# Kernel tuning notes

Hardware: AMD Instinct MI355X
Metric: run time of the kernel (lower is better)

## Reference

```python
import jax, jax.numpy as jnp
import numpy as np

PLANE_SIZE = 512
FEATURE_DIM = 8
N_LEVELS = 8
MULTISCALE = [1, 2, 4]
LOG2_PS = 9.0  # log2(plane_size)
N_SAMPLES = 1 << 20


def _build_pyramid(tex):
    # tex: [3, R, R, C] -> (flat [3, T, C], sizes [L], offsets [L]) via 2x2 box-filter mips
    levels = [tex]
    t = tex
    for _ in range(N_LEVELS - 1):
        P, h, w, C = t.shape
        t = t.reshape(P, h // 2, 2, w // 2, 2, C).mean(axis=(2, 4))
        levels.append(t)
    sizes = np.array([l.shape[1] for l in levels], dtype=np.int32)
    offsets = np.array([0] + list(np.cumsum(sizes.astype(np.int64) ** 2)[:-1]), dtype=np.int32)
    flat = jnp.concatenate([l.reshape(l.shape[0], -1, l.shape[-1]) for l in levels], axis=1)
    return flat, jnp.asarray(sizes), jnp.asarray(offsets)


def _bilinear_at_level(flat, sizes, offsets, uv, lvl_idx):
    # flat: [3, T, C]; uv: [3, N, 2] in [0,1]; lvl_idx: [3, N] int32
    szi = sizes[lvl_idx]                      # [3, N]
    sz = szi.astype(uv.dtype)
    px = uv[..., 0] * sz - 0.5                # texel centers at (i+0.5)/sz
    py = uv[..., 1] * sz - 0.5
    x0 = jnp.floor(px)
    y0 = jnp.floor(py)
    fx = (px - x0)[..., None]
    fy = (py - y0)[..., None]
    x0i = jnp.clip(x0.astype(jnp.int32), 0, szi - 1)
    x1i = jnp.clip(x0.astype(jnp.int32) + 1, 0, szi - 1)
    y0i = jnp.clip(y0.astype(jnp.int32), 0, szi - 1)
    y1i = jnp.clip(y0.astype(jnp.int32) + 1, 0, szi - 1)
    base = offsets[lvl_idx]

    def gather(yi, xi):
        idx = base + yi * szi + xi            # [3, N]
        return jax.vmap(lambda t, i: t[i])(flat, idx)  # [3, N, C]

    v00 = gather(y0i, x0i)
    v01 = gather(y0i, x1i)
    v10 = gather(y1i, x0i)
    v11 = gather(y1i, x1i)
    top = v00 * (1.0 - fx) + v01 * fx
    bot = v10 * (1.0 - fx) + v11 * fx
    return top * (1.0 - fy) + bot * fy


def _texture(grid, uv, bias):
    # mip-biased trilinear lookup (nvdiffrast linear-mipmap-linear, clamp boundary)
    flat, sizes, offsets = _build_pyramid(grid)
    max_mip = N_LEVELS - 1
    lvl = jnp.clip(bias, 0.0, float(max_mip))
    l0 = jnp.floor(lvl).astype(jnp.int32)
    l1 = jnp.minimum(l0 + 1, max_mip)
    f = (lvl - l0.astype(lvl.dtype))[..., None]
    s0 = _bilinear_at_level(flat, sizes, offsets, uv, l0)
    s1 = _bilinear_at_level(flat, sizes, offsets, uv, l1)
    return s0 * (1.0 - f) + s1 * f            # [3, N, C]


def _forward(x, level, grids):
    n = x.shape[0]
    uv = jnp.stack([x[:, [1, 2]], x[:, [0, 2]], x[:, [0, 1]]], axis=0)  # [3, N, 2]
    lvl = jnp.broadcast_to(level[:, 0][None, :], (3, n))                # [3, N]
    outs = []
    for s, g in enumerate(grids):
        enc = _texture(g, uv, lvl + LOG2_PS + float(s))                 # [3, N, C]
        outs.append(jnp.transpose(enc, (1, 0, 2)).reshape(n, 3 * FEATURE_DIM))
    return jnp.concatenate(outs, axis=-1)     # [N, 3*C*n_scales]


def setup_inputs() -> dict:
    key = jax.random.key(0)
    ks = jax.random.split(key, 5)
    x = jax.random.uniform(ks[0], (N_SAMPLES, 3), dtype=jnp.float32)
    # per-sample LOD so that bias = level + log2(plane_size) + scale spans the mip pyramid
    level = jax.random.uniform(ks[1], (N_SAMPLES, 1), dtype=jnp.float32) * (N_LEVELS - 1) - LOG2_PS
    inp = {"x": x, "level": level}
    for s, mult in enumerate(MULTISCALE):
        r = PLANE_SIZE * mult
        inp[f"grid{s}"] = jax.random.uniform(ks[2 + s], (3, r, r, FEATURE_DIM), jnp.float32, -0.01, 0.01)
    return inp


def reference(x, level, grid0, grid1, grid2):
    return _forward(x, level, (grid0, grid1, grid2))
```

## Files before the change

kernel.cpp:

```cpp
#include <hip/hip_runtime.h>

#define BLK 256
#define SBLK 192
#define NBIN 4096
#define NB 256


#define T0 0
#define T1 1048560
#define T2 2097072
#define TEX_TOTAL 3145392

__device__ __forceinline__ unsigned bfrne(float x) {
    unsigned u = __float_as_uint(x);
    return (u + 0x7fffu + ((u >> 16) & 1u)) >> 16;
}

__device__ __forceinline__ uint4 pack8(const float o[8]) {
    uint4 q;
    q.x = bfrne(o[0]) | (bfrne(o[1]) << 16);
    q.y = bfrne(o[2]) | (bfrne(o[3]) << 16);
    q.z = bfrne(o[4]) | (bfrne(o[5]) << 16);
    q.w = bfrne(o[6]) | (bfrne(o[7]) << 16);
    return q;
}

__device__ __forceinline__ void dec8(const uint4 q, float o[8]) {
    o[0] = __uint_as_float(q.x << 16);
    o[1] = __uint_as_float(q.x & 0xffff0000u);
    o[2] = __uint_as_float(q.y << 16);
    o[3] = __uint_as_float(q.y & 0xffff0000u);
    o[4] = __uint_as_float(q.z << 16);
    o[5] = __uint_as_float(q.z & 0xffff0000u);
    o[6] = __uint_as_float(q.w << 16);
    o[7] = __uint_as_float(q.w & 0xffff0000u);
}

__device__ __forceinline__ void acc8(const uint4 q, float w, float o[8]) {
    o[0] = fmaf(__uint_as_float(q.x << 16), w, o[0]);
    o[1] = fmaf(__uint_as_float(q.x & 0xffff0000u), w, o[1]);
    o[2] = fmaf(__uint_as_float(q.y << 16), w, o[2]);
    o[3] = fmaf(__uint_as_float(q.y & 0xffff0000u), w, o[3]);
    o[4] = fmaf(__uint_as_float(q.z << 16), w, o[4]);
    o[5] = fmaf(__uint_as_float(q.z & 0xffff0000u), w, o[5]);
    o[6] = fmaf(__uint_as_float(q.w << 16), w, o[6]);
    o[7] = fmaf(__uint_as_float(q.w & 0xffff0000u), w, o[7]);
}

__device__ __forceinline__ unsigned spread3(unsigned v) {
    return (v & 1u) | ((v & 2u) << 2) | ((v & 4u) << 4);
}

__device__ __forceinline__ unsigned mkey(float a, float b, float c, float lev) {
    int il = (int)(lev + 9.0f); il = min(max(il, 0), 7);
    int ia = (int)(a * 8.0f); ia = min(max(ia, 0), 7);
    int ib = (int)(b * 8.0f); ib = min(max(ib, 0), 7);
    int ic = (int)(c * 8.0f); ic = min(max(ic, 0), 7);
    unsigned m = (spread3((unsigned)ia) << 2) | (spread3((unsigned)ib) << 1) | spread3((unsigned)ic);
    return (m << 3) | (unsigned)il;
}

__global__ void __launch_bounds__(BLK) base_hist_kernel(
    const float* __restrict__ g0, const float* __restrict__ g1,
    const float* __restrict__ g2, uint4* __restrict__ wsT,
    const float* __restrict__ x, const float* __restrict__ level,
    unsigned* __restrict__ counts,
    int bA, int bB, int bC, int bBase, int n, int chunk) {
    if ((int)blockIdx.x >= bBase) {
        __shared__ unsigned h[NBIN];
        for (int b = threadIdx.x; b < NBIN; b += BLK) h[b] = 0;
        __syncthreads();
        int blk = blockIdx.x - bBase;
        int lo = blk * chunk, hi = min(lo + chunk, n);
        for (int i = lo + (int)threadIdx.x; i < hi; i += BLK) {
            unsigned key = mkey(x[3 * i], x[3 * i + 1], x[3 * i + 2], level[i]);
            atomicAdd(&h[key], 1u);
        }
        __syncthreads();
        for (int b = threadIdx.x; b < NBIN; b += BLK)
            counts[(size_t)b * NB + blk] = h[b];
        return;
    }
    int j = blockIdx.x * BLK + threadIdx.x;
    if (j >= bC) return;
    if (j < bA) {
        const float4* sp = (const float4*)g0 + (size_t)j * 2;
        float4 a = sp[0], b = sp[1];
        float o[8] = {a.x, a.y, a.z, a.w, b.x, b.y, b.z, b.w};
        wsT[T0 + j] = pack8(o);
    } else if (j < bB) {
        int t = j - bA;
        int p = t >> 18;
        int rem = t & ((1 << 18) - 1);
        int y = rem >> 9;
        int x2 = rem & 511;
        const float4* sp = (const float4*)g1 + (size_t)p * 1024 * 1024 * 2;
        float o[8] = {0, 0, 0, 0, 0, 0, 0, 0};
#pragma unroll
        for (int dy = 0; dy < 2; ++dy) {
#pragma unroll
            for (int dx = 0; dx < 2; ++dx) {
                size_t idx = ((size_t)(2 * y + dy) * 1024 + (2 * x2 + dx)) * 2;
                float4 a = sp[idx], b = sp[idx + 1];
                o[0] += a.x; o[1] += a.y; o[2] += a.z; o[3] += a.w;
                o[4] += b.x; o[5] += b.y; o[6] += b.z; o[7] += b.w;
            }
        }
#pragma unroll
        for (int c = 0; c < 8; ++c) o[c] *= 0.25f;
        wsT[T1 + t] = pack8(o);
    } else {
        int t = j - bB;
        int p = t >> 18;
        int rem = t & ((1 << 18) - 1);
        int y = rem >> 9;
        int x2 = rem & 511;
        const float4* sp = (const float4*)g2 + (size_t)p * 2048 * 2048 * 2;
        float o[8] = {0, 0, 0, 0, 0, 0, 0, 0};
#pragma unroll
        for (int dy = 0; dy < 4; ++dy) {
#pragma unroll
            for (int dx = 0; dx < 4; ++dx) {
                size_t idx = ((size_t)(4 * y + dy) * 2048 + (4 * x2 + dx)) * 2;
                float4 a = sp[idx], b = sp[idx + 1];
                o[0] += a.x; o[1] += a.y; o[2] += a.z; o[3] += a.w;
                o[4] += b.x; o[5] += b.y; o[6] += b.z; o[7] += b.w;
            }
        }
#pragma unroll
        for (int c = 0; c < 8; ++c) o[c] *= 0.0625f;
        wsT[T2 + t] = pack8(o);
    }
}

__global__ void __launch_bounds__(BLK) down2b_kernel(
    uint4* __restrict__ wsT,
    int srcA, int dstA, int lszA, int bA,
    int srcB, int dstB, int lszB, int bB,
    int srcC, int dstC, int lszC, int bC) {
    int j = blockIdx.x * BLK + threadIdx.x;
    if (j >= bC) return;
    int src, dst, lsz;
    if (j < bA) {
        src = srcA; dst = dstA; lsz = lszA;
    } else if (j < bB) {
        src = srcB; dst = dstB; lsz = lszB; j -= bA;
    } else {
        src = srcC; dst = dstC; lsz = lszC; j -= bB;
    }
    int sz = 1 << lsz;
    int p = j >> (2 * lsz);
    int rem = j & (sz * sz - 1);
    int y = rem >> lsz;
    int x = rem & (sz - 1);
    int S = sz << 1;
    const uint4* sp = wsT + src + (size_t)p * S * S;
    size_t i00 = (size_t)(2 * y) * S + 2 * x;
    float d0[8], d1[8], d2[8], d3[8];
    dec8(sp[i00], d0);
    dec8(sp[i00 + 1], d1);
    dec8(sp[i00 + S], d2);
    dec8(sp[i00 + S + 1], d3);
    float o[8];
#pragma unroll
    for (int c = 0; c < 8; ++c) o[c] = (d0[c] + d1[c] + d2[c] + d3[c]) * 0.25f;
    wsT[dst + (size_t)(p << (2 * lsz)) + rem] = pack8(o);
}

__global__ void __launch_bounds__(NB) scanA_kernel(
    unsigned* __restrict__ counts, unsigned* __restrict__ binTotal) {
    __shared__ unsigned tmp[NB];
    int bin = blockIdx.x, t = threadIdx.x;
    unsigned v = counts[(size_t)bin * NB + t];
    tmp[t] = v;
    __syncthreads();
    for (int d = 1; d < NB; d <<= 1) {
        unsigned u = (t >= d) ? tmp[t - d] : 0u;
        __syncthreads();
        tmp[t] += u;
        __syncthreads();
    }
    counts[(size_t)bin * NB + t] = tmp[t] - v;
    if (t == NB - 1) binTotal[bin] = tmp[t];
}

__global__ void __launch_bounds__(1024) scanB_kernel(
    const unsigned* __restrict__ binTotal, unsigned* __restrict__ binBase) {
    __shared__ unsigned tmp[1024];
    int t = threadIdx.x;
    unsigned v0 = binTotal[4 * t];
    unsigned v1 = binTotal[4 * t + 1];
    unsigned v2 = binTotal[4 * t + 2];
    unsigned v3 = binTotal[4 * t + 3];
    unsigned sum = v0 + v1 + v2 + v3;
    tmp[t] = sum;
    __syncthreads();
    for (int d = 1; d < 1024; d <<= 1) {
        unsigned u = (t >= d) ? tmp[t - d] : 0u;
        __syncthreads();
        tmp[t] += u;
        __syncthreads();
    }
    unsigned base = tmp[t] - sum;
    binBase[4 * t] = base;
    binBase[4 * t + 1] = base + v0;
    binBase[4 * t + 2] = base + v0 + v1;
    binBase[4 * t + 3] = base + v0 + v1 + v2;
}

__global__ void __launch_bounds__(BLK) scatter_kernel(
    const float* __restrict__ x, const float* __restrict__ level,
    const unsigned* __restrict__ prefix, const unsigned* __restrict__ binBase,
    float4* __restrict__ xs, unsigned* __restrict__ perm, int n, int chunk) {
    __shared__ unsigned h[NBIN];
    for (int b = threadIdx.x; b < NBIN; b += BLK) h[b] = 0;
    __syncthreads();
    int blk = blockIdx.x;
    int lo = blk * chunk, hi = min(lo + chunk, n);
    for (int i = lo + (int)threadIdx.x; i < hi; i += BLK) {
        float a = x[3 * i], b = x[3 * i + 1], c = x[3 * i + 2];
        float lv = level[i];
        unsigned key = mkey(a, b, c, lv);
        unsigned r = atomicAdd(&h[key], 1u);
        unsigned pos = binBase[key] + prefix[(size_t)key * NB + blk] + r;
        xs[pos] = make_float4(a, b, c, lv);
        perm[pos] = (unsigned)i;
    }
}

__device__ __forceinline__ void addr4(const uint4* __restrict__ t, int sz,
                                      float u, float v,
                                      const uint4** a, float* w) {
    float fsz = (float)sz;
    float px = u * fsz - 0.5f;
    float py = v * fsz - 0.5f;
    float x0f = floorf(px), y0f = floorf(py);
    float fx = px - x0f, fy = py - y0f;
    int xi = (int)x0f, yi = (int)y0f;
    int m = sz - 1;
    int x0 = min(max(xi, 0), m);
    int x1 = min(max(xi + 1, 0), m);
    int y0 = min(max(yi, 0), m);
    int y1 = min(max(yi + 1, 0), m);
    const uint4* r0 = t + (size_t)y0 * sz;
    const uint4* r1 = t + (size_t)y1 * sz;
    a[0] = r0 + x0;
    a[1] = r0 + x1;
    a[2] = r1 + x0;
    a[3] = r1 + x1;
    w[0] = (1.0f - fx) * (1.0f - fy);
    w[1] = fx * (1.0f - fy);
    w[2] = (1.0f - fx) * fy;
    w[3] = fx * fy;
}

__global__ void __launch_bounds__(SBLK) tex_sample_kernel(
    const float4* __restrict__ xs, const unsigned* __restrict__ perm,
    const uint4* __restrict__ wsT, float* __restrict__ out, int n) {
    __shared__ float so[3][64][25];
    __shared__ unsigned soi[64];
    int nblk = gridDim.x;
    int cpx = nblk >> 3;
    int bid = blockIdx.x;
    int bswz = (bid & 7) * cpx + (bid >> 3);
    int lane = threadIdx.x & 63;
    int s = threadIdx.x >> 6;
    int base = bswz * 64;
    int j = base + lane;
    bool valid = j < n;

    if (valid) {
        float4 xl = xs[j];
        float xv0 = xl.x, xv1 = xl.y, xv2 = xl.z, lev = xl.w;
        if (s == 0) soi[lane] = perm[j];

        const int WSS_[3] = {T0, T1, T2};
        const int OFFMIN_[3] = {0, 1048576, 5242880};

        const int R = 512 << s;
        float bias = lev + 9.0f + (float)s;
        float lvl = fminf(fmaxf(bias, 0.0f), 7.0f);
        float l0f = floorf(lvl);
        int l0 = (int)l0f;
        int l1 = min(l0 + 1, 7);
        float f = lvl - l0f;
        int sz0 = R >> l0;
        int sz1 = R >> l1;
        int off0 = ((R * R - sz0 * sz0) * 4) / 3;
        int off1 = ((R * R - sz1 * sz1) * 4) / 3;
        const uint4* base0 = wsT + WSS_[s] + (size_t)3 * (off0 - OFFMIN_[s]);
        const uint4* base1 = wsT + WSS_[s] + (size_t)3 * (off1 - OFFMIN_[s]);

        const uint4* ap[24];
        float w[6][4];
#pragma unroll
        for (int p = 0; p < 3; ++p) {
            float u = (p == 0) ? xv1 : xv0;
            float v = (p == 2) ? xv1 : xv2;
            addr4(base0 + (size_t)p * (sz0 * sz0), sz0, u, v, &ap[8 * p], w[2 * p]);
            addr4(base1 + (size_t)p * (sz1 * sz1), sz1, u, v, &ap[8 * p + 4], w[2 * p + 1]);
        }
        uint4 q[24];
#pragma unroll
        for (int t = 0; t < 24; ++t) q[t] = *ap[t];

        float omf = 1.0f - f;
#pragma unroll
        for (int p = 0; p < 3; ++p) {
            float a[8] = {0, 0, 0, 0, 0, 0, 0, 0};
            float b[8] = {0, 0, 0, 0, 0, 0, 0, 0};
#pragma unroll
            for (int t = 0; t < 4; ++t) acc8(q[8 * p + t], w[2 * p][t], a);
#pragma unroll
            for (int t = 0; t < 4; ++t) acc8(q[8 * p + 4 + t], w[2 * p + 1][t], b);
#pragma unroll
            for (int c = 0; c < 8; ++c)
                so[s][lane][8 * p + c] = a[c] * omf + b[c] * f;
        }
    }
    __syncthreads();
    if (valid) {
#pragma unroll
        for (int k = 0; k < 6; ++k) {
            int e = k * 64 + lane;
            int sample = (e * 10923) >> 16;
            int word = e - 6 * sample;
            if (base + sample < n) {
                float4 v;
                v.x = so[s][sample][word * 4 + 0];
                v.y = so[s][sample][word * 4 + 1];
                v.z = so[s][sample][word * 4 + 2];
                v.w = so[s][sample][word * 4 + 3];
                *(float4*)(out + (size_t)soi[sample] * 72 + s * 24 + word * 4) = v;
            }
        }
    }
}

extern "C" void kernel_launch(void* const* d_in, const int* in_sizes, int n_in,
                              void* d_out, int out_size, void* d_ws, size_t ws_size,
                              hipStream_t stream) {
    const float* x = (const float*)d_in[0];
    const float* level = (const float*)d_in[1];
    const float* g0 = (const float*)d_in[2];
    const float* g1 = (const float*)d_in[3];
    const float* g2 = (const float*)d_in[4];
    float* out = (float*)d_out;
    uint4* wsT = (uint4*)d_ws;
    int n = in_sizes[0] / 3;

    float4* xs = (float4*)(wsT + TEX_TOTAL);
    unsigned* perm = (unsigned*)(xs + n);
    unsigned* counts = perm + n;
    unsigned* binTotal = counts + (size_t)NBIN * NB;
    unsigned* binBase = binTotal + NBIN;

    auto lvlOff = [](int s, int l) -> int {
        const int WSS[3] = {T0, T1, T2};
        const int OFFMIN[3] = {0, 1048576, 5242880};
        int R = 512 << s;
        int sz = R >> l;
        int off = ((R * R - sz * sz) * 4) / 3;
        return WSS[s] + 3 * (off - OFFMIN[s]);
    };

    int chunk = (n + NB - 1) / NB;

    {
        int bA = 3 * 512 * 512;
        int bB = bA * 2;
        int bC = bA * 3;
        int bBase = (bC + BLK - 1) / BLK;
        base_hist_kernel<<<bBase + NB, BLK, 0, stream>>>(
            g0, g1, g2, wsT, x, level, counts, bA, bB, bC, bBase, n, chunk);
    }
    for (int l = 1; l <= 7; ++l) {
        int szA = 512 >> l;
        int bA = 3 * szA * szA;
        int srcA = lvlOff(0, l - 1), dstA = lvlOff(0, l), lszA = 9 - l;
        int bB = bA, srcB = 0, dstB = 0, lszB = 0;
        int bC = bA, srcC = 0, dstC = 0, lszC = 0;
        if (l >= 2) {
            int szB = 1024 >> l;
            bB = bA + 3 * szB * szB;
            srcB = lvlOff(1, l - 1); dstB = lvlOff(1, l); lszB = 10 - l;
            bC = bB;
        }
        if (l >= 3) {
            int szC = 2048 >> l;
            bC = bB + 3 * szC * szC;
            srcC = lvlOff(2, l - 1); dstC = lvlOff(2, l); lszC = 11 - l;
        }
        down2b_kernel<<<(bC + BLK - 1) / BLK, BLK, 0, stream>>>(
            wsT, srcA, dstA, lszA, bA, srcB, dstB, lszB, bB, srcC, dstC, lszC, bC);
    }

    scanA_kernel<<<NBIN, NB, 0, stream>>>(counts, binTotal);
    scanB_kernel<<<1, 1024, 0, stream>>>(binTotal, binBase);
    scatter_kernel<<<NB, BLK, 0, stream>>>(x, level, counts, binBase, xs, perm, n, chunk);

    int nblk = (n + 63) / 64;
    nblk = (nblk + 7) & ~7;
    tex_sample_kernel<<<nblk, SBLK, 0, stream>>>(xs, perm, wsT, out, n);
}
```

Before: 412.6 us.

## Fuse mip downsample levels into scan/scatter kernels; split sampler per plane

```diff
diff --git a/kernel.cpp b/kernel.cpp
--- a/kernel.cpp
+++ b/kernel.cpp
@@ -1,7 +1,7 @@
 #include <hip/hip_runtime.h>
 
 #define BLK 256
-#define SBLK 192
+#define SBLK 576
 #define NBIN 4096
 #define NB 256
 
@@ -133,12 +133,11 @@
     }
 }
 
-__global__ void __launch_bounds__(BLK) down2b_kernel(
-    uint4* __restrict__ wsT,
+__device__ __forceinline__ void down2b_body(
+    uint4* __restrict__ wsT, int j,
     int srcA, int dstA, int lszA, int bA,
     int srcB, int dstB, int lszB, int bB,
     int srcC, int dstC, int lszC, int bC) {
-    int j = blockIdx.x * BLK + threadIdx.x;
     if (j >= bC) return;
     int src, dst, lsz;
     if (j < bA) {
@@ -167,65 +166,104 @@
     wsT[dst + (size_t)(p << (2 * lsz)) + rem] = pack8(o);
 }
 
-__global__ void __launch_bounds__(NB) scanA_kernel(
-    unsigned* __restrict__ counts, unsigned* __restrict__ binTotal) {
-    __shared__ unsigned tmp[NB];
-    int bin = blockIdx.x, t = threadIdx.x;
-    unsigned v = counts[(size_t)bin * NB + t];
-    tmp[t] = v;
-    __syncthreads();
-    for (int d = 1; d < NB; d <<= 1) {
-        unsigned u = (t >= d) ? tmp[t - d] : 0u;
+__global__ void __launch_bounds__(BLK) down2b_kernel(
+    uint4* __restrict__ wsT,
+    int srcA, int dstA, int lszA, int bA,
+    int srcB, int dstB, int lszB, int bB,
+    int srcC, int dstC, int lszC, int bC) {
+    down2b_body(wsT, blockIdx.x * BLK + threadIdx.x,
+                srcA, dstA, lszA, bA, srcB, dstB, lszB, bB, srcC, dstC, lszC, bC);
+}
+
+__global__ void __launch_bounds__(BLK) scanA_down_kernel(
+    uint4* __restrict__ wsT, unsigned* __restrict__ counts,
+    unsigned* __restrict__ binTotal, int nScan,
+    int srcA, int dstA, int lszA, int bA,
+    int srcB, int dstB, int lszB, int bB,
+    int srcC, int dstC, int lszC, int bC) {
+    if ((int)blockIdx.x < nScan) {
+        __shared__ unsigned tmp[NB];
+        int bin = blockIdx.x, t = threadIdx.x;
+        unsigned v = counts[(size_t)bin * NB + t];
+        tmp[t] = v;
         __syncthreads();
-        tmp[t] += u;
+        for (int d = 1; d < NB; d <<= 1) {
+            unsigned u = (t >= d) ? tmp[t - d] : 0u;
+            __syncthreads();
+            tmp[t] += u;
+            __syncthreads();
+        }
+        counts[(size_t)bin * NB + t] = tmp[t] - v;
+        if (t == NB - 1) binTotal[bin] = tmp[t];
+        return;
+    }
+    down2b_body(wsT, (blockIdx.x - nScan) * BLK + threadIdx.x,
+                srcA, dstA, lszA, bA, srcB, dstB, lszB, bB, srcC, dstC, lszC, bC);
+}
+
+__global__ void __launch_bounds__(BLK) scanB_down_kernel(
+    uint4* __restrict__ wsT, const unsigned* __restrict__ binTotal,
+    unsigned* __restrict__ binBase,
+    int srcA, int dstA, int lszA, int bA,
+    int srcB, int dstB, int lszB, int bB,
+    int srcC, int dstC, int lszC, int bC) {
+    if (blockIdx.x == 0) {
+        __shared__ unsigned tmp[BLK];
+        int t = threadIdx.x;
+        unsigned v[16];
+        unsigned sum = 0;
+#pragma unroll
+        for (int k = 0; k < 16; ++k) {
+            v[k] = binTotal[t * 16 + k];
+            sum += v[k];
+        }
+        tmp[t] = sum;
         __syncthreads();
-    }
-    counts[(size_t)bin * NB + t] = tmp[t] - v;
-    if (t == NB - 1) binTotal[bin] = tmp[t];
-}
-
-__global__ void __launch_bounds__(1024) scanB_kernel(
-    const unsigned* __restrict__ binTotal, unsigned* __restrict__ binBase) {
-    __shared__ unsigned tmp[1024];
-    int t = threadIdx.x;
-    unsigned v0 = binTotal[4 * t];
-    unsigned v1 = binTotal[4 * t + 1];
-    unsigned v2 = binTotal[4 * t + 2];
-    unsigned v3 = binTotal[4 * t + 3];
-    unsigned sum = v0 + v1 + v2 + v3;
-    tmp[t] = sum;
-    __syncthreads();
-    for (int d = 1; d < 1024; d <<= 1) {
-        unsigned u = (t >= d) ? tmp[t - d] : 0u;
-        __syncthreads();
-        tmp[t] += u;
-        __syncthreads();
-    }
-    unsigned base = tmp[t] - sum;
-    binBase[4 * t] = base;
-    binBase[4 * t + 1] = base + v0;
-    binBase[4 * t + 2] = base + v0 + v1;
-    binBase[4 * t + 3] = base + v0 + v1 + v2;
-}
-
-__global__ void __launch_bounds__(BLK) scatter_kernel(
+        for (int d = 1; d < BLK; d <<= 1) {
+            unsigned u = (t >= d) ? tmp[t - d] : 0u;
+            __syncthreads();
+            tmp[t] += u;
+            __syncthreads();
+        }
+        unsigned run = tmp[t] - sum;
+#pragma unroll
+        for (int k = 0; k < 16; ++k) {
+            binBase[t * 16 + k] = run;
+            run += v[k];
+        }
+        return;
+    }
+    down2b_body(wsT, (blockIdx.x - 1) * BLK + threadIdx.x,
+                srcA, dstA, lszA, bA, srcB, dstB, lszB, bB, srcC, dstC, lszC, bC);
+}
+
+__global__ void __launch_bounds__(BLK) scatter_down_kernel(
+    uint4* __restrict__ wsT,
     const float* __restrict__ x, const float* __restrict__ level,
     const unsigned* __restrict__ prefix, const unsigned* __restrict__ binBase,
-    float4* __restrict__ xs, unsigned* __restrict__ perm, int n, int chunk) {
-    __shared__ unsigned h[NBIN];
-    for (int b = threadIdx.x; b < NBIN; b += BLK) h[b] = 0;
-    __syncthreads();
-    int blk = blockIdx.x;
-    int lo = blk * chunk, hi = min(lo + chunk, n);
-    for (int i = lo + (int)threadIdx.x; i < hi; i += BLK) {
-        float a = x[3 * i], b = x[3 * i + 1], c = x[3 * i + 2];
-        float lv = level[i];
-        unsigned key = mkey(a, b, c, lv);
-        unsigned r = atomicAdd(&h[key], 1u);
-        unsigned pos = binBase[key] + prefix[(size_t)key * NB + blk] + r;
-        xs[pos] = make_float4(a, b, c, lv);
-        perm[pos] = (unsigned)i;
-    }
+    float4* __restrict__ xs, unsigned* __restrict__ perm, int n, int chunk,
+    int srcA, int dstA, int lszA, int bA,
+    int srcB, int dstB, int lszB, int bB,
+    int srcC, int dstC, int lszC, int bC) {
+    if ((int)blockIdx.x < NB) {
+        __shared__ unsigned h[NBIN];
+        for (int b = threadIdx.x; b < NBIN; b += BLK) h[b] = 0;
+        __syncthreads();
+        int blk = blockIdx.x;
+        int lo = blk * chunk, hi = min(lo + chunk, n);
+        for (int i = lo + (int)threadIdx.x; i < hi; i += BLK) {
+            float a = x[3 * i], b = x[3 * i + 1], c = x[3 * i + 2];
+            float lv = level[i];
+            unsigned key = mkey(a, b, c, lv);
+            unsigned r = atomicAdd(&h[key], 1u);
+            unsigned pos = binBase[key] + prefix[(size_t)key * NB + blk] + r;
+            xs[pos] = make_float4(a, b, c, lv);
+            perm[pos] = (unsigned)i;
+        }
+        return;
+    }
+    down2b_body(wsT, (blockIdx.x - NB) * BLK + threadIdx.x,
+                srcA, dstA, lszA, bA, srcB, dstB, lszB, bB, srcC, dstC, lszC, bC);
 }
 
 __device__ __forceinline__ void addr4(const uint4* __restrict__ t, int sz,
@@ -257,28 +295,30 @@
 __global__ void __launch_bounds__(SBLK) tex_sample_kernel(
     const float4* __restrict__ xs, const unsigned* __restrict__ perm,
     const uint4* __restrict__ wsT, float* __restrict__ out, int n) {
-    __shared__ float so[3][64][25];
+    __shared__ float so[64][75];
     __shared__ unsigned soi[64];
     int nblk = gridDim.x;
     int cpx = nblk >> 3;
     int bid = blockIdx.x;
     int bswz = (bid & 7) * cpx + (bid >> 3);
+    int base = bswz * 64;
+    if (base >= n) return;
     int lane = threadIdx.x & 63;
-    int s = threadIdx.x >> 6;
-    int base = bswz * 64;
+    int wv = threadIdx.x >> 6;
+    int s = (wv * 11) >> 5;
+    int p = wv - 3 * s;
     int j = base + lane;
     bool valid = j < n;
 
     if (valid) {
         float4 xl = xs[j];
-        float xv0 = xl.x, xv1 = xl.y, xv2 = xl.z, lev = xl.w;
-        if (s == 0) soi[lane] = perm[j];
+        if (wv == 0) soi[lane] = perm[j];
 
         const int WSS_[3] = {T0, T1, T2};
         const int OFFMIN_[3] = {0, 1048576, 5242880};
 
         const int R = 512 << s;
-        float bias = lev + 9.0f + (float)s;
+        float bias = xl.w + 9.0f + (float)s;
         float lvl = fminf(fmaxf(bias, 0.0f), 7.0f);
         float l0f = floorf(lvl);
         int l0 = (int)l0f;
@@ -291,48 +331,43 @@
         const uint4* base0 = wsT + WSS_[s] + (size_t)3 * (off0 - OFFMIN_[s]);
         const uint4* base1 = wsT + WSS_[s] + (size_t)3 * (off1 - OFFMIN_[s]);
 
-        const uint4* ap[24];
-        float w[6][4];
-#pragma unroll
-        for (int p = 0; p < 3; ++p) {
-            float u = (p == 0) ? xv1 : xv0;
-            float v = (p == 2) ? xv1 : xv2;
-            addr4(base0 + (size_t)p * (sz0 * sz0), sz0, u, v, &ap[8 * p], w[2 * p]);
-            addr4(base1 + (size_t)p * (sz1 * sz1), sz1, u, v, &ap[8 * p + 4], w[2 * p + 1]);
-        }
-        uint4 q[24];
-#pragma unroll
-        for (int t = 0; t < 24; ++t) q[t] = *ap[t];
-
+        float u = (p == 0) ? xl.y : xl.x;
+        float v = (p == 2) ? xl.y : xl.z;
+        const uint4* ap[8];
+        float w0[4], w1[4];
+        addr4(base0 + (size_t)p * (sz0 * sz0), sz0, u, v, &ap[0], w0);
+        addr4(base1 + (size_t)p * (sz1 * sz1), sz1, u, v, &ap[4], w1);
+        uint4 q[8];
+#pragma unroll
+        for (int t = 0; t < 8; ++t) q[t] = *ap[t];
+
+        float a[8] = {0, 0, 0, 0, 0, 0, 0, 0};
+        float b[8] = {0, 0, 0, 0, 0, 0, 0, 0};
+#pragma unroll
+        for (int t = 0; t < 4; ++t) acc8(q[t], w0[t], a);
+#pragma unroll
+        for (int t = 0; t < 4; ++t) acc8(q[4 + t], w1[t], b);
         float omf = 1.0f - f;
-#pragma unroll
-        for (int p = 0; p < 3; ++p) {
-            float a[8] = {0, 0, 0, 0, 0, 0, 0, 0};
-            float b[8] = {0, 0, 0, 0, 0, 0, 0, 0};
-#pragma unroll
-            for (int t = 0; t < 4; ++t) acc8(q[8 * p + t], w[2 * p][t], a);
-#pragma unroll
-            for (int t = 0; t < 4; ++t) acc8(q[8 * p + 4 + t], w[2 * p + 1][t], b);
-#pragma unroll
-            for (int c = 0; c < 8; ++c)
-                so[s][lane][8 * p + c] = a[c] * omf + b[c] * f;
-        }
+        int c0 = s * 24 + p * 8;
+#pragma unroll
+        for (int c = 0; c < 8; ++c)
+            so[lane][c0 + c] = a[c] * omf + b[c] * f;
     }
     __syncthreads();
-    if (valid) {
-#pragma unroll
-        for (int k = 0; k < 6; ++k) {
-            int e = k * 64 + lane;
-            int sample = (e * 10923) >> 16;
-            int word = e - 6 * sample;
-            if (base + sample < n) {
-                float4 v;
-                v.x = so[s][sample][word * 4 + 0];
-                v.y = so[s][sample][word * 4 + 1];
-                v.z = so[s][sample][word * 4 + 2];
-                v.w = so[s][sample][word * 4 + 3];
-                *(float4*)(out + (size_t)soi[sample] * 72 + s * 24 + word * 4) = v;
-            }
+    int nsmp = min(64, n - base);
+    int lim = nsmp * 18;
+#pragma unroll
+    for (int k = 0; k < 2; ++k) {
+        int e = k * SBLK + (int)threadIdx.x;
+        if (e < lim) {
+            int sample = (e * 3641) >> 16;
+            int word = e - 18 * sample;
+            float4 v;
+            v.x = so[sample][word * 4 + 0];
+            v.y = so[sample][word * 4 + 1];
+            v.z = so[sample][word * 4 + 2];
+            v.w = so[sample][word * 4 + 3];
+            *(float4*)(out + (size_t)soi[sample] * 72 + word * 4) = v;
         }
     }
 }
@@ -374,12 +409,15 @@
         base_hist_kernel<<<bBase + NB, BLK, 0, stream>>>(
             g0, g1, g2, wsT, x, level, counts, bA, bB, bC, bBase, n, chunk);
     }
-    for (int l = 1; l <= 7; ++l) {
+
+    auto segs = [&](int l, int& srcA, int& dstA, int& lszA, int& bA,
+                    int& srcB, int& dstB, int& lszB, int& bB,
+                    int& srcC, int& dstC, int& lszC, int& bC) {
         int szA = 512 >> l;
-        int bA = 3 * szA * szA;
-        int srcA = lvlOff(0, l - 1), dstA = lvlOff(0, l), lszA = 9 - l;
-        int bB = bA, srcB = 0, dstB = 0, lszB = 0;
-        int bC = bA, srcC = 0, dstC = 0, lszC = 0;
+        bA = 3 * szA * szA;
+        srcA = lvlOff(0, l - 1); dstA = lvlOff(0, l); lszA = 9 - l;
+        bB = bA; srcB = 0; dstB = 0; lszB = 0;
+        bC = bA; srcC = 0; dstC = 0; lszC = 0;
         if (l >= 2) {
             int szB = 1024 >> l;
             bB = bA + 3 * szB * szB;
@@ -391,13 +429,36 @@
             bC = bB + 3 * szC * szC;
             srcC = lvlOff(2, l - 1); dstC = lvlOff(2, l); lszC = 11 - l;
         }
+    };
+
+    int srcA, dstA, lszA, bA, srcB, dstB, lszB, bB, srcC, dstC, lszC, bC;
+
+    segs(1, srcA, dstA, lszA, bA, srcB, dstB, lszB, bB, srcC, dstC, lszC, bC);
+    {
+        int nDown = (bC + BLK - 1) / BLK;
+        scanA_down_kernel<<<NBIN + nDown, BLK, 0, stream>>>(
+            wsT, counts, binTotal, NBIN,
+            srcA, dstA, lszA, bA, srcB, dstB, lszB, bB, srcC, dstC, lszC, bC);
+    }
+    segs(2, srcA, dstA, lszA, bA, srcB, dstB, lszB, bB, srcC, dstC, lszC, bC);
+    {
+        int nDown = (bC + BLK - 1) / BLK;
+        scanB_down_kernel<<<1 + nDown, BLK, 0, stream>>>(
+            wsT, binTotal, binBase,
+            srcA, dstA, lszA, bA, srcB, dstB, lszB, bB, srcC, dstC, lszC, bC);
+    }
+    segs(3, srcA, dstA, lszA, bA, srcB, dstB, lszB, bB, srcC, dstC, lszC, bC);
+    {
+        int nDown = (bC + BLK - 1) / BLK;
+        scatter_down_kernel<<<NB + nDown, BLK, 0, stream>>>(
+            wsT, x, level, counts, binBase, xs, perm, n, chunk,
+            srcA, dstA, lszA, bA, srcB, dstB, lszB, bB, srcC, dstC, lszC, bC);
+    }
+    for (int l = 4; l <= 7; ++l) {
+        segs(l, srcA, dstA, lszA, bA, srcB, dstB, lszB, bB, srcC, dstC, lszC, bC);
         down2b_kernel<<<(bC + BLK - 1) / BLK, BLK, 0, stream>>>(
             wsT, srcA, dstA, lszA, bA, srcB, dstB, lszB, bB, srcC, dstC, lszC, bC);
     }
-
-    scanA_kernel<<<NBIN, NB, 0, stream>>>(counts, binTotal);
-    scanB_kernel<<<1, 1024, 0, stream>>>(binTotal, binBase);
-    scatter_kernel<<<NB, BLK, 0, stream>>>(x, level, counts, binBase, xs, perm, n, chunk);
 
     int nblk = (n + 63) / 64;
     nblk = (nblk + 7) & ~7;
```

New measurement: 422.0 us. +2.3%, slower.
